# Kernel optimization log

Measured on AMD Instinct MI355X. Metric: run time of the kernel, lower is better.

Reference implementation:

```python
import jax, jax.numpy as jnp
import numpy as np

N = 50000          # nodes
E = 800000         # edges
F_IN = 128         # node_features
HID = 128          # hidden_dim
OUT = 64           # out_channels
TOP = 4            # top_features (gate channels)
EXP = 3            # experts
G = 64             # num graphs in batch
TEMP = 101.0       # 100 - 0/(200*0.01) + final_temperature(1.0) at batch counter 0


def setup_inputs() -> dict:
    key = jax.random.key(0)
    ks = jax.random.split(key, 12)
    s = 0.08  # weight init scale
    x = jax.random.normal(ks[0], (N, F_IN), jnp.float32)
    top_features = jax.random.normal(ks[1], (N, TOP), jnp.float32)
    edge_index = jax.random.randint(ks[2], (2, E), 0, N, dtype=jnp.int64)
    batch = jnp.sort(jax.random.randint(ks[3], (N,), 0, G, dtype=jnp.int64))
    W0 = jax.random.normal(ks[4], (EXP, F_IN, HID), jnp.float32) * s
    b0 = jax.random.normal(ks[5], (EXP, HID), jnp.float32) * s
    Wg0 = jax.random.normal(ks[6], (EXP, TOP), jnp.float32) * s
    W1 = jax.random.normal(ks[7], (EXP, HID, HID), jnp.float32) * s
    b1 = jax.random.normal(ks[8], (EXP, HID), jnp.float32) * s
    Wg1 = jax.random.normal(ks[9], (EXP, TOP), jnp.float32) * s
    Wf = jax.random.normal(ks[10], (HID, OUT), jnp.float32) * s
    bf = jax.random.normal(ks[11], (OUT,), jnp.float32) * s
    return {"x": x, "top_features": top_features, "edge_index": edge_index,
            "batch": batch, "W0": W0, "b0": b0, "Wg0": Wg0,
            "W1": W1, "b1": b1, "Wg1": Wg1, "Wf": Wf, "bf": bf}


def reference(x, top_features, edge_index, batch, W0, b0, Wg0, W1, b1, Wg1, Wf, bf):
    # GCN with self-loops and symmetric normalization (PyG GCNConv default)
    sl = jnp.arange(N, dtype=edge_index.dtype)
    src = jnp.concatenate([edge_index[0], sl])
    dst = jnp.concatenate([edge_index[1], sl])
    deg = jax.ops.segment_sum(jnp.ones_like(src, jnp.float32), dst, num_segments=N)
    dinv = jax.lax.rsqrt(deg)  # deg >= 1 thanks to self loops
    norm = dinv[src] * dinv[dst]  # [E+N]

    def camoe_layer(h, W, b, Wg):
        # gate: softmax over experts at temperature TEMP
        gate = jax.nn.softmax((top_features @ Wg.T) / TEMP, axis=-1)  # [N, EXP]
        out = jnp.zeros((N, W.shape[2]), h.dtype)
        for e in range(EXP):  # small fixed expert loop (keeps peak memory low)
            he = h @ W[e]                                            # [N, HID]
            agg = jax.ops.segment_sum(he[src] * norm[:, None], dst, num_segments=N)
            out = out + gate[:, e:e + 1] * jax.nn.relu(agg + b[e])
        return out

    h = camoe_layer(x, W0, b0, Wg0)
    # F.dropout before last layer: eval mode -> identity
    h = camoe_layer(h, W1, b1, Wg1)

    # global mean pool over graphs
    sums = jax.ops.segment_sum(h, batch, num_segments=G)             # [G, HID]
    cnt = jax.ops.segment_sum(jnp.ones((N,), h.dtype), batch, num_segments=G)
    pooled = sums / jnp.maximum(cnt, 1.0)[:, None]
    return pooled @ Wf + bf                                          # [G, OUT]
```

## Files before the change

### kernel.cpp

```cpp
#include <hip/hip_runtime.h>
#include <hip/hip_bf16.h>

#define HID 128
#define EXP 3
#define TOP 4
#define OUTC 64

typedef __bf16 bf16x8 __attribute__((ext_vector_type(8)));
typedef float f32x16 __attribute__((ext_vector_type(16)));
typedef float f32x2 __attribute__((ext_vector_type(2)));

#define GLDS_STRIDE 272
#define OUT_STRIDE 132
#define ECAP 2048

__device__ __forceinline__ unsigned int pack4_fp8(float a, float b, float c, float d) {
    int v = 0;
    v = __builtin_amdgcn_cvt_pk_fp8_f32(a, b, v, false);
    v = __builtin_amdgcn_cvt_pk_fp8_f32(c, d, v, true);
    return (unsigned int)v;
}

__device__ __forceinline__ void unpack4_fp8(unsigned int v, float* out) {
    f32x2 lo = __builtin_amdgcn_cvt_pk_f32_fp8((int)v, false);
    f32x2 hi = __builtin_amdgcn_cvt_pk_f32_fp8((int)v, true);
    out[0] = lo[0]; out[1] = lo[1]; out[2] = hi[0]; out[3] = hi[1];
}

__device__ __forceinline__ void fma16_fp8(uint4 a, float w, float* acc) {
    unsigned int q[4] = {a.x, a.y, a.z, a.w};
#pragma unroll
    for (int k = 0; k < 4; ++k) {
        float f[4];
        unpack4_fp8(q[k], f);
#pragma unroll
        for (int j = 0; j < 4; ++j) acc[k * 4 + j] += f[j] * w;
    }
}


__global__ __launch_bounds__(256) void mega0_kernel(
        const int* __restrict__ dst, int* __restrict__ cnt, int E,
        const float* __restrict__ x, unsigned int* __restrict__ x8,
        const float* __restrict__ tf, const float* __restrict__ Wg0,
        const float* __restrict__ Wg1, float* __restrict__ gates,
        const int* __restrict__ batch, int* __restrict__ gstart,
        const float* __restrict__ W0, const float* __restrict__ W1,
        __bf16* __restrict__ ph0, __bf16* __restrict__ ph1,
        int N, int G, int nCount, int nConv, int nGate) {
    int b = blockIdx.x;
    int t = threadIdx.x;

    if (b < nCount) {
        int slice = b & 7;
        int base = (b >> 3) * 2048 + t * 8;
        if (base < E) {
            if (base + 8 <= E) {
                int4 d0 = *(const int4*)(dst + base);
                int4 d1 = *(const int4*)(dst + base + 4);
                int dv[8] = {d0.x, d0.y, d0.z, d0.w, d1.x, d1.y, d1.z, d1.w};
#pragma unroll
                for (int k = 0; k < 8; ++k)
                    if (((dv[k] >> 6) & 7) == slice) atomicAdd(&cnt[dv[k]], 1);
            } else {
                for (int i = base; i < E; ++i) {
                    int d = dst[i];
                    if (((d >> 6) & 7) == slice) atomicAdd(&cnt[d], 1);
                }
            }
        }
        return;
    }
    b -= nCount;
    if (b < nConv) {
        int i = b * 256 + t;
        int total16 = N * (HID / 16);
        if (i < total16) {
            const float4* xp = (const float4*)x + (size_t)i * 4;
            float4 v0 = xp[0], v1 = xp[1], v2 = xp[2], v3 = xp[3];
            uint4 o;
            o.x = pack4_fp8(v0.x, v0.y, v0.z, v0.w);
            o.y = pack4_fp8(v1.x, v1.y, v1.z, v1.w);
            o.z = pack4_fp8(v2.x, v2.y, v2.z, v2.w);
            o.w = pack4_fp8(v3.x, v3.y, v3.z, v3.w);
            ((uint4*)x8)[i] = o;
        }
        return;
    }
    b -= nConv;
    if (b < nGate) {
        int n = b * 256 + t;
        if (n >= N) return;
        float4 tv = *(const float4*)(tf + (size_t)n * TOP);
        const float* Wg[2] = {Wg0, Wg1};
#pragma unroll
        for (int l = 0; l < 2; ++l) {
            float lg[EXP];
#pragma unroll
            for (int e = 0; e < EXP; ++e) {
                const float* w = Wg[l] + e * TOP;
                lg[e] = (tv.x * w[0] + tv.y * w[1] + tv.z * w[2] + tv.w * w[3]) * (1.0f / 101.0f);
            }
            float m = fmaxf(lg[0], fmaxf(lg[1], lg[2]));
            float e0 = expf(lg[0] - m), e1 = expf(lg[1] - m), e2 = expf(lg[2] - m);
            float inv = 1.0f / (e0 + e1 + e2);
            gates[n * 6 + l * 3 + 0] = e0 * inv;
            gates[n * 6 + l * 3 + 1] = e1 * inv;
            gates[n * 6 + l * 3 + 2] = e2 * inv;
        }
        return;
    }
    b -= nGate;
    if (b == 0) {
        int g = t;
        if (g > G) return;
        if (g == G) { gstart[G] = N; return; }
        int lo = 0, hi = N;
        while (lo < hi) {
            int mid = (lo + hi) >> 1;
            if (batch[mid] < g) lo = mid + 1; else hi = mid;
        }
        gstart[g] = lo;
        return;
    }
    b -= 1;
    int job = b * 4 + (t >> 6);
    if (job >= 192) return;
    int l = t & 63;
    int layer = job / 96;
    int rem = job % 96;
    int e = rem / 32;
    int s = (rem % 32) / 4;
    int c = rem % 4;
    const float* W = layer ? W1 : W0;
    __bf16* ph = layer ? ph1 : ph0;
    size_t dstbase = (size_t)((((e * 8 + s) * 4 + c) * 64 + l)) * 8;
    int kbase = s * 16 + (l >> 5) * 8;
    int ncol = c * 32 + (l & 31);
#pragma unroll
    for (int j = 0; j < 8; ++j) {
        float w = W[(size_t)e * (HID * HID) + (size_t)(kbase + j) * HID + ncol];
        ph[dstbase + j] = (__bf16)w;
    }
}


__global__ __launch_bounds__(256) void scan_local_kernel(const int* __restrict__ cnt,
                                                         int* __restrict__ row_ptr,
                                                         int* __restrict__ bsum,
                                                         float* __restrict__ dinv, int N) {
    __shared__ int sh[256];
    int b = blockIdx.x;
    int t = threadIdx.x;
    int base = b * 1024 + t * 4;
    int v[4] = {0, 0, 0, 0};
    if (base + 3 < N) {
        int4 c = *(const int4*)(cnt + base);
        v[0] = c.x; v[1] = c.y; v[2] = c.z; v[3] = c.w;
    } else {
#pragma unroll
        for (int k = 0; k < 4; ++k) if (base + k < N) v[k] = cnt[base + k];
    }
#pragma unroll
    for (int k = 0; k < 4; ++k)
        if (base + k < N) dinv[base + k] = rsqrtf((float)v[k] + 1.0f);
    int s = v[0] + v[1] + v[2] + v[3];
    sh[t] = s;
    __syncthreads();
    for (int off = 1; off < 256; off <<= 1) {
        int u = (t >= off) ? sh[t - off] : 0;
        __syncthreads();
        sh[t] += u;
        __syncthreads();
    }
    int run = sh[t] - s;
#pragma unroll
    for (int k = 0; k < 4; ++k) {
        if (base + k < N) row_ptr[base + k] = run;
        run += v[k];
    }
    if (t == 255) bsum[b] = sh[255];
}

__global__ __launch_bounds__(256) void scan_fixup2_kernel(const int* __restrict__ bsum, int nb,
                                                          int* __restrict__ row_ptr,
                                                          int* __restrict__ cursor, int N) {
    __shared__ int soff;
    int b = blockIdx.x;
    int t = threadIdx.x;
    if (t < 64) {
        int v = 0;
        for (int j = t; j < b; j += 64) v += bsum[j];
#pragma unroll
        for (int k = 1; k < 64; k <<= 1) v += __shfl_xor(v, k, 64);
        if (t == 0) soff = v;
    }
    __syncthreads();
    int off = soff;
    int base = b * 1024 + t * 4;
#pragma unroll
    for (int k = 0; k < 4; ++k) {
        int i = base + k;
        if (i < N) {
            int r = row_ptr[i] + off;
            row_ptr[i] = r;
            cursor[i] = r;
        }
    }
    if (b == nb - 1 && t == 0) row_ptr[N] = off + bsum[b];
}

__global__ __launch_bounds__(256) void fill_kernel(const int* __restrict__ src,
                                                   const int* __restrict__ dst,
                                                   int* __restrict__ cursor,
                                                   const float* __restrict__ dinv,
                                                   int2* __restrict__ erec, int E) {
    int b = blockIdx.x;
    int slice = b & 7;
    int base = (b >> 3) * 2048 + threadIdx.x * 8;
    if (base >= E) return;
    if (base + 8 <= E) {
        int4 d0 = *(const int4*)(dst + base);
        int4 d1 = *(const int4*)(dst + base + 4);
        int dv[8] = {d0.x, d0.y, d0.z, d0.w, d1.x, d1.y, d1.z, d1.w};
#pragma unroll
        for (int k = 0; k < 8; ++k) {
            int d = dv[k];
            if (((d >> 6) & 7) != slice) continue;
            int s = src[base + k];
            int p = atomicAdd(&cursor[d], 1);
            erec[p] = make_int2(s, __float_as_int(dinv[s] * dinv[d]));
        }
    } else {
        for (int i = base; i < E; ++i) {
            int d = dst[i];
            if (((d >> 6) & 7) != slice) continue;
            int s = src[i];
            int p = atomicAdd(&cursor[d], 1);
            erec[p] = make_int2(s, __float_as_int(dinv[s] * dinv[d]));
        }
    }
}


__global__ __launch_bounds__(512, 4) void fused_layer_kernel(
        const unsigned char* __restrict__ h8in,
        const __bf16* __restrict__ wpkh,
        const float* __restrict__ bias, const float* __restrict__ gates, int gate_off,
        const int* __restrict__ row_ptr, const int2* __restrict__ erec,
        const float* __restrict__ dinv,
        unsigned char* __restrict__ hout8,
        const int* __restrict__ batch, float* __restrict__ pooled, int N) {
    __shared__ char lds[64 * OUT_STRIDE * 4];
    int tid = threadIdx.x;
    int row0 = blockIdx.x * 64;

    int2* ecache = (int2*)(lds + 64 * GLDS_STRIDE);

    int rows = min(64, N - row0);
    int s_blk = row_ptr[row0];
    int e_blk = row_ptr[row0 + rows];
    int ecnt = min(e_blk - s_blk, ECAP);
    for (int i = tid; i < ecnt; i += 512) ecache[i] = erec[s_blk + i];
    __syncthreads();

    {
        int r = tid >> 3;
        int part = tid & 7;
        int n = row0 + r;
        float acc[16];
#pragma unroll
        for (int j = 0; j < 16; ++j) acc[j] = 0.f;
        if (n < N) {
            const unsigned char* hb = h8in + part * 16;
            int s = row_ptr[n], e = row_ptr[n + 1];
            uint4 v = *(const uint4*)(hb + (size_t)n * HID);
            float dn = dinv[n];
            float ws = dn * dn;
            {
                unsigned int q[4] = {v.x, v.y, v.z, v.w};
#pragma unroll
                for (int k = 0; k < 4; ++k) {
                    float f[4];
                    unpack4_fp8(q[k], f);
#pragma unroll
                    for (int j = 0; j < 4; ++j) acc[k * 4 + j] = f[j] * ws;
                }
            }
            if (e - s_blk <= ECAP) {
                const int2* ep = ecache - s_blk;
                int i = s;
                for (; i + 3 < e; i += 4) {
                    int2 r0 = ep[i], r1 = ep[i + 1], r2 = ep[i + 2], r3 = ep[i + 3];
                    uint4 a0 = *(const uint4*)(hb + (size_t)r0.x * HID);
                    uint4 a1 = *(const uint4*)(hb + (size_t)r1.x * HID);
                    uint4 a2 = *(const uint4*)(hb + (size_t)r2.x * HID);
                    uint4 a3 = *(const uint4*)(hb + (size_t)r3.x * HID);
                    fma16_fp8(a0, __int_as_float(r0.y), acc);
                    fma16_fp8(a1, __int_as_float(r1.y), acc);
                    fma16_fp8(a2, __int_as_float(r2.y), acc);
                    fma16_fp8(a3, __int_as_float(r3.y), acc);
                }
                for (; i < e; ++i) {
                    int2 r0 = ep[i];
                    uint4 a0 = *(const uint4*)(hb + (size_t)r0.x * HID);
                    fma16_fp8(a0, __int_as_float(r0.y), acc);
                }
            } else {
                int i = s;
                for (; i + 3 < e; i += 4) {
                    int2 r0 = erec[i], r1 = erec[i + 1], r2 = erec[i + 2], r3 = erec[i + 3];
                    uint4 a0 = *(const uint4*)(hb + (size_t)r0.x * HID);
                    uint4 a1 = *(const uint4*)(hb + (size_t)r1.x * HID);
                    uint4 a2 = *(const uint4*)(hb + (size_t)r2.x * HID);
                    uint4 a3 = *(const uint4*)(hb + (size_t)r3.x * HID);
                    fma16_fp8(a0, __int_as_float(r0.y), acc);
                    fma16_fp8(a1, __int_as_float(r1.y), acc);
                    fma16_fp8(a2, __int_as_float(r2.y), acc);
                    fma16_fp8(a3, __int_as_float(r3.y), acc);
                }
                for (; i < e; ++i) {
                    int2 r0 = erec[i];
                    uint4 a0 = *(const uint4*)(hb + (size_t)r0.x * HID);
                    fma16_fp8(a0, __int_as_float(r0.y), acc);
                }
            }
        }
        char* drow = lds + r * GLDS_STRIDE + part * 32;
        bf16x8 h0, h1;
#pragma unroll
        for (int j = 0; j < 8; ++j) { h0[j] = (__bf16)acc[j]; h1[j] = (__bf16)acc[8 + j]; }
        *(bf16x8*)drow = h0;
        *(bf16x8*)(drow + 16) = h1;
    }
    __syncthreads();

    int lane = tid & 63;
    int wave = tid >> 6;
    int m = lane & 31;
    int g = lane >> 5;
    int rhalf = wave & 1;
    int cq = wave >> 1;
    const char* arow = lds + (rhalf * 32 + m) * GLDS_STRIDE + g * 16;
    int rowbase = row0 + rhalf * 32 + 4 * g;

    float F[16];
#pragma unroll
    for (int r = 0; r < 16; ++r) F[r] = 0.f;

    for (int e = 0; e < EXP; ++e) {
        f32x16 acc;
#pragma unroll
        for (int r = 0; r < 16; ++r) acc[r] = 0.f;

#pragma unroll
        for (int s = 0; s < 8; ++s) {
            bf16x8 Ah = *(const bf16x8*)(arow + s * 32);
            bf16x8 Bh = *(const bf16x8*)(wpkh + (size_t)(((e * 8 + s) * 4 + cq) * 64 + lane) * 8);
            acc = __builtin_amdgcn_mfma_f32_32x32x16_bf16(Ah, Bh, acc, 0, 0, 0);
        }
        float gt[16];
#pragma unroll
        for (int r = 0; r < 16; ++r) {
            int rr = rowbase + (r & 3) + 8 * (r >> 2);
            gt[r] = (rr < N) ? gates[(size_t)rr * 6 + gate_off + e] : 0.f;
        }
        float bb = bias[e * HID + cq * 32 + m];
#pragma unroll
        for (int r = 0; r < 16; ++r)
            F[r] += gt[r] * fmaxf(acc[r] + bb, 0.f);
    }

    __syncthreads();
    float* lds32 = (float*)lds;
    {
        int colg = cq * 32 + m;
#pragma unroll
        for (int r = 0; r < 16; ++r) {
            int lr = rhalf * 32 + 4 * g + (r & 3) + 8 * (r >> 2);
            lds32[lr * OUT_STRIDE + colg] = F[r];
        }
    }
    __syncthreads();

    if (hout8) {
#pragma unroll
        for (int it = 0; it < 4; ++it) {
            int id = tid + it * 512;
            int r = id >> 5;
            int c4 = id & 31;
            int gr = row0 + r;
            if (gr < N) {
                const float* src = &lds32[r * OUT_STRIDE + c4 * 4];
                *(unsigned int*)(hout8 + (size_t)gr * HID + c4 * 4) =
                    pack4_fp8(src[0], src[1], src[2], src[3]);
            }
        }
    }
    if (pooled) {
        int col = tid & 127;
        int rbase = (tid >> 7) * 16;
        int cur = -1;
        float acc = 0.f;
        for (int r = 0; r < 16; ++r) {
            int gr = row0 + rbase + r;
            if (gr >= N) break;
            int gb = batch[gr];
            if (gb != cur) {
                if (cur >= 0) atomicAdd(&pooled[cur * HID + col], acc);
                acc = 0.f;
                cur = gb;
            }
            acc += lds32[(rbase + r) * OUT_STRIDE + col];
        }
        if (cur >= 0) atomicAdd(&pooled[cur * HID + col], acc);
    }
}


__global__ __launch_bounds__(64) void final_kernel(const float* __restrict__ pooled,
                                                   const int* __restrict__ gstart,
                                                   const float* __restrict__ Wf,
                                                   const float* __restrict__ bf,
                                                   float* __restrict__ out) {
    __shared__ float ps[HID];
    int g = blockIdx.x;
    int o = threadIdx.x;
    float invc = 1.0f / fmaxf((float)(gstart[g + 1] - gstart[g]), 1.0f);
    ps[o] = pooled[g * HID + o] * invc;
    ps[o + 64] = pooled[g * HID + o + 64] * invc;
    __syncthreads();
    float acc = bf[o];
#pragma unroll 8
    for (int k = 0; k < HID; ++k) acc = fmaf(ps[k], Wf[k * OUTC + o], acc);
    out[g * OUTC + o] = acc;
}


extern "C" void kernel_launch(void* const* d_in, const int* in_sizes, int n_in,
                              void* d_out, int out_size, void* d_ws, size_t ws_size,
                              hipStream_t stream) {
    const float* x   = (const float*)d_in[0];
    const float* tf  = (const float*)d_in[1];
    const int*   ei  = (const int*)d_in[2];
    const int*   bat = (const int*)d_in[3];
    const float* W0  = (const float*)d_in[4];
    const float* b0  = (const float*)d_in[5];
    const float* Wg0 = (const float*)d_in[6];
    const float* W1  = (const float*)d_in[7];
    const float* b1  = (const float*)d_in[8];
    const float* Wg1 = (const float*)d_in[9];
    const float* Wf  = (const float*)d_in[10];
    const float* bf  = (const float*)d_in[11];
    float* out = (float*)d_out;

    const int N = in_sizes[0] / HID;
    const int E = in_sizes[2] / 2;
    const int G = out_size / OUTC;
    const int NB = (N + 1023) / 1024;

    char* p = (char*)d_ws;
    auto alloc = [&](size_t bytes) -> void* {
        void* r = (void*)p;
        p += (bytes + 255) & ~(size_t)255;
        return r;
    };
    int*           cnt    = (int*)alloc((size_t)N * 4);
    float*         pooled = (float*)alloc((size_t)G * HID * 4);
    float*         dinv   = (float*)alloc((size_t)N * 4);
    int*           rowp   = (int*)alloc((size_t)(N + 1) * 4);
    int*           cursor = (int*)alloc((size_t)N * 4);
    float*         gates  = (float*)alloc((size_t)N * 6 * 4);
    int2*          erec   = (int2*)alloc((size_t)E * 8);
    unsigned char* x8     = (unsigned char*)alloc((size_t)N * HID);
    unsigned char* h8b    = (unsigned char*)alloc((size_t)N * HID);
    int*           gstart = (int*)alloc((size_t)(G + 1) * 4);
    int*           bsum   = (int*)alloc((size_t)NB * 4);
    __bf16*        wpkh0  = (__bf16*)alloc((size_t)EXP * HID * HID * 2);
    __bf16*        wpkh1  = (__bf16*)alloc((size_t)EXP * HID * HID * 2);

    const int* src = ei;
    const int* dst = ei + E;

    size_t zlen = (size_t)((char*)pooled - (char*)cnt) + (size_t)G * HID * 4;
    hipMemsetAsync(cnt, 0, zlen, stream);

    const int nCount = ((E + 2047) / 2048) * 8;
    const int nConv = (N * (HID / 16) + 255) / 256;
    const int nGate = (N + 255) / 256;
    const int megaBlocks = nCount + nConv + nGate + 1 + 48;

    mega0_kernel<<<megaBlocks, 256, 0, stream>>>(dst, cnt, E,
                                                 x, (unsigned int*)x8,
                                                 tf, Wg0, Wg1, gates,
                                                 bat, gstart,
                                                 W0, W1, wpkh0, wpkh1,
                                                 N, G, nCount, nConv, nGate);
    scan_local_kernel<<<NB, 256, 0, stream>>>(cnt, rowp, bsum, dinv, N);
    scan_fixup2_kernel<<<NB, 256, 0, stream>>>(bsum, NB, rowp, cursor, N);
    fill_kernel<<<nCount, 256, 0, stream>>>(src, dst, cursor, dinv, erec, E);

    int gemm_blocks = (N + 63) / 64;

    fused_layer_kernel<<<gemm_blocks, 512, 0, stream>>>(x8, wpkh0, b0, gates, 0,
                                                        rowp, erec, dinv,
                                                        h8b, nullptr, nullptr, N);
    fused_layer_kernel<<<gemm_blocks, 512, 0, stream>>>(h8b, wpkh1, b1, gates, 3,
                                                        rowp, erec, dinv,
                                                        nullptr, bat, pooled, N);

    final_kernel<<<G, 64, 0, stream>>>(pooled, gstart, Wf, bf, out);
}
```

Measured before the change: 261.0 us.

## Split degree counters and CSR cursors into eight copies to cut atomic contention

Degree counting and CSR fill now spread their atomics over eight per-lane-class copies of the counter and cursor arrays instead of one shared array. The scan sums the copies to get degrees, and the fixup writes per-copy starting cursors as a prefix within each node's row. This is meant to reduce same-address atomic contention during counting and filling. In exchange it costs eight times the counter memory, a larger memset, and more reads in the scan kernels. The copy a thread uses is chosen the same way in count and fill, so the row layout stays consistent.

After: 255.0 us. 2.3% less time.

```diff
diff --git a/kernel.cpp b/kernel.cpp
--- a/kernel.cpp
+++ b/kernel.cpp
@@ -5,6 +5,7 @@
 #define EXP 3
 #define TOP 4
 #define OUTC 64
+#define NCPY 8
 
 typedef __bf16 bf16x8 __attribute__((ext_vector_type(8)));
 typedef float f32x16 __attribute__((ext_vector_type(16)));
@@ -40,7 +41,7 @@
 
 
 __global__ __launch_bounds__(256) void mega0_kernel(
-        const int* __restrict__ dst, int* __restrict__ cnt, int E,
+        const int* __restrict__ dst, int* __restrict__ cnt8, int E,
         const float* __restrict__ x, unsigned int* __restrict__ x8,
         const float* __restrict__ tf, const float* __restrict__ Wg0,
         const float* __restrict__ Wg1, float* __restrict__ gates,
@@ -56,16 +57,19 @@
         int base = (b >> 3) * 2048 + t * 8;
         if (base < E) {
             if (base + 8 <= E) {
+                int cls = t & 7;
+                int* cc = cnt8 + cls * N;
                 int4 d0 = *(const int4*)(dst + base);
                 int4 d1 = *(const int4*)(dst + base + 4);
                 int dv[8] = {d0.x, d0.y, d0.z, d0.w, d1.x, d1.y, d1.z, d1.w};
 #pragma unroll
                 for (int k = 0; k < 8; ++k)
-                    if (((dv[k] >> 6) & 7) == slice) atomicAdd(&cnt[dv[k]], 1);
+                    if (((dv[k] >> 6) & 7) == slice) atomicAdd(&cc[dv[k]], 1);
             } else {
                 for (int i = base; i < E; ++i) {
                     int d = dst[i];
-                    if (((d >> 6) & 7) == slice) atomicAdd(&cnt[d], 1);
+                    if (((d >> 6) & 7) == slice)
+                        atomicAdd(&cnt8[((i >> 3) & 7) * N + d], 1);
                 }
             }
         }
@@ -145,7 +149,7 @@
 }
 
 
-__global__ __launch_bounds__(256) void scan_local_kernel(const int* __restrict__ cnt,
+__global__ __launch_bounds__(256) void scan_local_kernel(const int* __restrict__ cnt8,
                                                          int* __restrict__ row_ptr,
                                                          int* __restrict__ bsum,
                                                          float* __restrict__ dinv, int N) {
@@ -155,11 +159,16 @@
     int base = b * 1024 + t * 4;
     int v[4] = {0, 0, 0, 0};
     if (base + 3 < N) {
-        int4 c = *(const int4*)(cnt + base);
-        v[0] = c.x; v[1] = c.y; v[2] = c.z; v[3] = c.w;
+#pragma unroll
+        for (int c = 0; c < NCPY; ++c) {
+            int4 cc = *(const int4*)(cnt8 + (size_t)c * N + base);
+            v[0] += cc.x; v[1] += cc.y; v[2] += cc.z; v[3] += cc.w;
+        }
     } else {
 #pragma unroll
-        for (int k = 0; k < 4; ++k) if (base + k < N) v[k] = cnt[base + k];
+        for (int k = 0; k < 4; ++k)
+            if (base + k < N)
+                for (int c = 0; c < NCPY; ++c) v[k] += cnt8[(size_t)c * N + base + k];
     }
 #pragma unroll
     for (int k = 0; k < 4; ++k)
@@ -184,7 +193,8 @@
 
 __global__ __launch_bounds__(256) void scan_fixup2_kernel(const int* __restrict__ bsum, int nb,
                                                           int* __restrict__ row_ptr,
-                                                          int* __restrict__ cursor, int N) {
+                                                          const int* __restrict__ cnt8,
+                                                          int* __restrict__ ccur, int N) {
     __shared__ int soff;
     int b = blockIdx.x;
     int t = threadIdx.x;
@@ -198,13 +208,28 @@
     __syncthreads();
     int off = soff;
     int base = b * 1024 + t * 4;
-#pragma unroll
-    for (int k = 0; k < 4; ++k) {
-        int i = base + k;
-        if (i < N) {
-            int r = row_ptr[i] + off;
-            row_ptr[i] = r;
-            cursor[i] = r;
+    if (base + 3 < N) {
+        int4 rp = *(const int4*)(row_ptr + base);
+        int pre[4] = {rp.x + off, rp.y + off, rp.z + off, rp.w + off};
+        *(int4*)(row_ptr + base) = make_int4(pre[0], pre[1], pre[2], pre[3]);
+#pragma unroll
+        for (int c = 0; c < NCPY; ++c) {
+            int4 cc = *(const int4*)(cnt8 + (size_t)c * N + base);
+            *(int4*)(ccur + (size_t)c * N + base) = make_int4(pre[0], pre[1], pre[2], pre[3]);
+            pre[0] += cc.x; pre[1] += cc.y; pre[2] += cc.z; pre[3] += cc.w;
+        }
+    } else {
+#pragma unroll
+        for (int k = 0; k < 4; ++k) {
+            int i = base + k;
+            if (i < N) {
+                int pre = row_ptr[i] + off;
+                row_ptr[i] = pre;
+                for (int c = 0; c < NCPY; ++c) {
+                    ccur[(size_t)c * N + i] = pre;
+                    pre += cnt8[(size_t)c * N + i];
+                }
+            }
         }
     }
     if (b == nb - 1 && t == 0) row_ptr[N] = off + bsum[b];
@@ -212,14 +237,16 @@
 
 __global__ __launch_bounds__(256) void fill_kernel(const int* __restrict__ src,
                                                    const int* __restrict__ dst,
-                                                   int* __restrict__ cursor,
+                                                   int* __restrict__ ccur,
                                                    const float* __restrict__ dinv,
-                                                   int2* __restrict__ erec, int E) {
+                                                   int2* __restrict__ erec, int E, int N) {
     int b = blockIdx.x;
     int slice = b & 7;
     int base = (b >> 3) * 2048 + threadIdx.x * 8;
     if (base >= E) return;
     if (base + 8 <= E) {
+        int cls = threadIdx.x & 7;
+        int* cc = ccur + cls * N;
         int4 d0 = *(const int4*)(dst + base);
         int4 d1 = *(const int4*)(dst + base + 4);
         int dv[8] = {d0.x, d0.y, d0.z, d0.w, d1.x, d1.y, d1.z, d1.w};
@@ -228,7 +255,7 @@
             int d = dv[k];
             if (((d >> 6) & 7) != slice) continue;
             int s = src[base + k];
-            int p = atomicAdd(&cursor[d], 1);
+            int p = atomicAdd(&cc[d], 1);
             erec[p] = make_int2(s, __float_as_int(dinv[s] * dinv[d]));
         }
     } else {
@@ -236,7 +263,7 @@
             int d = dst[i];
             if (((d >> 6) & 7) != slice) continue;
             int s = src[i];
-            int p = atomicAdd(&cursor[d], 1);
+            int p = atomicAdd(&ccur[((i >> 3) & 7) * N + d], 1);
             erec[p] = make_int2(s, __float_as_int(dinv[s] * dinv[d]));
         }
     }
@@ -465,11 +492,11 @@
         p += (bytes + 255) & ~(size_t)255;
         return r;
     };
-    int*           cnt    = (int*)alloc((size_t)N * 4);
+    int*           cnt8   = (int*)alloc((size_t)NCPY * N * 4);
     float*         pooled = (float*)alloc((size_t)G * HID * 4);
+    int*           ccur   = (int*)alloc((size_t)NCPY * N * 4);
     float*         dinv   = (float*)alloc((size_t)N * 4);
     int*           rowp   = (int*)alloc((size_t)(N + 1) * 4);
-    int*           cursor = (int*)alloc((size_t)N * 4);
     float*         gates  = (float*)alloc((size_t)N * 6 * 4);
     int2*          erec   = (int2*)alloc((size_t)E * 8);
     unsigned char* x8     = (unsigned char*)alloc((size_t)N * HID);
@@ -482,23 +509,23 @@
     const int* src = ei;
     const int* dst = ei + E;
 
-    size_t zlen = (size_t)((char*)pooled - (char*)cnt) + (size_t)G * HID * 4;
-    hipMemsetAsync(cnt, 0, zlen, stream);
+    size_t zlen = (size_t)((char*)pooled - (char*)cnt8) + (size_t)G * HID * 4;
+    hipMemsetAsync(cnt8, 0, zlen, stream);
 
     const int nCount = ((E + 2047) / 2048) * 8;
     const int nConv = (N * (HID / 16) + 255) / 256;
     const int nGate = (N + 255) / 256;
     const int megaBlocks = nCount + nConv + nGate + 1 + 48;
 
-    mega0_kernel<<<megaBlocks, 256, 0, stream>>>(dst, cnt, E,
+    mega0_kernel<<<megaBlocks, 256, 0, stream>>>(dst, cnt8, E,
                                                  x, (unsigned int*)x8,
                                                  tf, Wg0, Wg1, gates,
                                                  bat, gstart,
                                                  W0, W1, wpkh0, wpkh1,
                                                  N, G, nCount, nConv, nGate);
-    scan_local_kernel<<<NB, 256, 0, stream>>>(cnt, rowp, bsum, dinv, N);
-    scan_fixup2_kernel<<<NB, 256, 0, stream>>>(bsum, NB, rowp, cursor, N);
-    fill_kernel<<<nCount, 256, 0, stream>>>(src, dst, cursor, dinv, erec, E);
+    scan_local_kernel<<<NB, 256, 0, stream>>>(cnt8, rowp, bsum, dinv, N);
+    scan_fixup2_kernel<<<NB, 256, 0, stream>>>(bsum, NB, rowp, cnt8, ccur, N);
+    fill_kernel<<<nCount, 256, 0, stream>>>(src, dst, ccur, dinv, erec, E, N);
 
     int gemm_blocks = (N + 63) / 64;
 
```
